# Optimization experiments

Hardware: AMD Instinct MI355X
Metric: run time of the kernel (lower is better)

## Reference

```python
import jax, jax.numpy as jnp
import numpy as np

B, N, M, F, K = 32, 256, 64, 128, 64
N_INTERACT_RES, N_ATOM_RES = 3, 2


def ssp(x):
    # shifted softplus, PhysNet activation
    return jax.nn.softplus(x) - jnp.log(2.0).astype(x.dtype)


def res_block(h, W1, b1, W2, b2):
    # PhysNet residual layer: h + W2 @ ssp(W1 @ ssp(h) + b1) + b2
    t = ssp(h)
    t = ssp(t @ W1.T + b1)
    return h + t @ W2.T + b2


def setup_inputs() -> dict:
    key = jax.random.key(0)
    ks = jax.random.split(key, 20)
    sF = 1.0 / np.sqrt(F)
    sK = 1.0 / np.sqrt(K)
    return {
        "x": jax.random.normal(ks[0], (B, N, F), jnp.float32),
        "rbf": jax.random.uniform(ks[1], (B, N, M, K), jnp.float32),
        "neighbor": jax.random.randint(ks[2], (B, N, M), 0, N, jnp.int32),
        "k2f_W": jax.random.normal(ks[3], (F, K), jnp.float32) * sK,  # no bias
        "Wi": jax.random.normal(ks[4], (F, F), jnp.float32) * sF,
        "bi": jnp.zeros((F,), jnp.float32),
        "ires_W1": jax.random.normal(ks[5], (N_INTERACT_RES, F, F), jnp.float32) * sF,
        "ires_b1": jnp.zeros((N_INTERACT_RES, F), jnp.float32),
        "ires_W2": jax.random.normal(ks[6], (N_INTERACT_RES, F, F), jnp.float32) * sF,
        "ires_b2": jnp.zeros((N_INTERACT_RES, F), jnp.float32),
        "Wint": jax.random.normal(ks[7], (F, F), jnp.float32) * sF,
        "bint": jnp.zeros((F,), jnp.float32),
        "u_gate": jnp.ones((F,), jnp.float32),
        "ares_W1": jax.random.normal(ks[8], (N_ATOM_RES, F, F), jnp.float32) * sF,
        "ares_b1": jnp.zeros((N_ATOM_RES, F), jnp.float32),
        "ares_W2": jax.random.normal(ks[9], (N_ATOM_RES, F, F), jnp.float32) * sF,
        "ares_b2": jnp.zeros((N_ATOM_RES, F), jnp.float32),
    }


def reference(x, rbf, neighbor, k2f_W, Wi, bi, ires_W1, ires_b1, ires_W2, ires_b2,
              Wint, bint, u_gate, ares_W1, ares_b1, ares_W2, ares_b2):
    b, n, f = x.shape
    m = neighbor.shape[2]
    xa = ssp(x)                                            # (B,N,F)
    g = jnp.einsum('bnmk,fk->bnmf', rbf, k2f_W)            # RBF filter (B,N,M,F)
    xi = ssp(xa @ Wi.T + bi)                               # self message
    # gather neighbor features: xj[b,n,m,:] = xa[b, neighbor[b,n,m], :]
    idx = jnp.broadcast_to(neighbor.reshape(b, n * m)[:, :, None], (b, n * m, f))
    xj = jnp.take_along_axis(xa, idx, axis=1).reshape(b, n, m, f)
    xj = jnp.sum(xj * g, axis=2)                           # aggregate over neighbors
    v = xi + xj
    for l in range(ires_W1.shape[0]):
        v = res_block(v, ires_W1[l], ires_b1[l], ires_W2[l], ires_b2[l])
    v = ssp(v)
    out = u_gate * x + (v @ Wint.T + bint)
    for l in range(ares_W1.shape[0]):
        out = res_block(out, ares_W1[l], ares_b1[l], ares_W2[l], ares_b2[l])
    return out
```

## Files before the change

### kernel.cpp

```cpp
#include <hip/hip_runtime.h>
#include <math.h>

#define PB 32
#define PN 256
#define PM 64
#define PF 128
#define PK 64
#define ROWS (PB*PN)
#define NTOT (ROWS*PF)

#define OFF_K2F  0
#define OFF_WI   8192
#define OFF_IW1  24576
#define OFF_IW2  73728
#define OFF_WINT 122880
#define OFF_AW1  139264
#define OFF_AW2  172032
#define TOTAL_W  204800

#define XPITCH 136
#define GPITCH 132

#define APB 32

typedef __attribute__((ext_vector_type(4))) float  floatx4;
typedef __attribute__((ext_vector_type(8))) short  shortx8;

__device__ __forceinline__ unsigned short f2b(float f){
    union { float f; unsigned int i; } c; c.f = f;
    unsigned int x = c.i;
    return (unsigned short)((x + 0x7fffu + ((x >> 16) & 1u)) >> 16);
}
__device__ __forceinline__ float sspf(float x){
    const float LOG2E = 1.4426950408889634f;
    const float LN2   = 0.6931471805599453f;
    float t = __builtin_amdgcn_exp2f(-fabsf(x) * LOG2E);
    return fmaxf(x, 0.0f) + LN2 * __builtin_amdgcn_logf(1.0f + t) - LN2;
}
__device__ __forceinline__ shortx8 pack8(float4 a, float4 b){
    shortx8 r;
    r[0]=(short)f2b(a.x); r[1]=(short)f2b(a.y); r[2]=(short)f2b(a.z); r[3]=(short)f2b(a.w);
    r[4]=(short)f2b(b.x); r[5]=(short)f2b(b.y); r[6]=(short)f2b(b.z); r[7]=(short)f2b(b.w);
    return r;
}

__global__ __launch_bounds__(256) void k_pre(const float* __restrict__ x,
                                             const float* __restrict__ k2f,
                                             const float* __restrict__ Wi,
                                             const float* __restrict__ iW1,
                                             const float* __restrict__ iW2,
                                             const float* __restrict__ Wint,
                                             const float* __restrict__ aW1,
                                             const float* __restrict__ aW2,
                                             float* __restrict__ xa_f,
                                             unsigned short* __restrict__ xa_b,
                                             unsigned short* __restrict__ Wb){
    int i = blockIdx.x * 256 + threadIdx.x;
    if (i < NTOT){
        float v = sspf(x[i]);
        xa_f[i] = v;
        xa_b[i] = f2b(v);
        return;
    }
    int j = i - NTOT;
    if (j >= TOTAL_W) return;
    float v;
    if      (j < OFF_WI)   v = k2f[j - OFF_K2F];
    else if (j < OFF_IW1)  v = Wi[j - OFF_WI];
    else if (j < OFF_IW2)  v = iW1[j - OFF_IW1];
    else if (j < OFF_WINT) v = iW2[j - OFF_IW2];
    else if (j < OFF_AW1)  v = Wint[j - OFF_WINT];
    else if (j < OFF_AW2)  v = aW1[j - OFF_AW1];
    else                   v = aW2[j - OFF_AW2];
    Wb[j] = f2b(v);
}

__global__ __launch_bounds__(512, 2) void k_msg(const float* __restrict__ rbf,
                                                const int* __restrict__ nbr,
                                                const unsigned short* __restrict__ Wk2f,
                                                const float* __restrict__ xa_f,
                                                float* __restrict__ xj){
    const int tid  = threadIdx.x;
    const int w    = tid >> 6;
    const int lane = tid & 63;
    const int quad = lane >> 4;
    const int l16  = lane & 15;

    const int blk   = blockIdx.x;
    const int b     = blk >> 3;
    const int atom0 = b * PN + (blk & 7) * APB;
    const int awave = atom0 + w*4;

    __shared__ float          xa_s[PN * GPITCH];
    __shared__ unsigned short w_s[8192];

    const int rboff = l16 * PK + quad*8;
    const float* rb_base = rbf + (size_t)awave * (PM*PK);
    const int*   nb_base = nbr + (size_t)awave * PM + quad*4;

    float4 r0, r1, r2, r3; int4 nb;
    {
        const float* p0 = rb_base + rboff;
        r0 = *(const float4*)(p0);
        r1 = *(const float4*)(p0 + 4);
        r2 = *(const float4*)(p0 + 32);
        r3 = *(const float4*)(p0 + 36);
        nb = *(const int4*)(nb_base);
    }

    #pragma unroll
    for (int rep = 0; rep < 2; ++rep){
        int f  = rep*512 + tid;
        int s  = f >> 9;
        int ft = (f >> 6) & 7;
        int ln = f & 63;
        const unsigned short* g = Wk2f + (size_t)(ft*16 + (ln & 15))*PK + s*32 + (ln >> 4)*8;
        *(shortx8*)(&w_s[f*8]) = *(const shortx8*)(g);
    }

    const float* src = xa_f + (size_t)b * (PN*PF);
    #pragma unroll
    for (int p = 0; p < 16; ++p){
        int idx = p*2048 + tid*4;
        int row = idx >> 7, col = idx & 127;
        *(float4*)(&xa_s[row*GPITCH + col]) = *(const float4*)(src + idx);
    }
    __syncthreads();

    float s[8];
    #pragma unroll
    for (int it = 0; it < 16; ++it){
        const int ai = it >> 2;
        const int t  = it & 3;

        shortx8 af0 = pack8(r0, r1);
        shortx8 af1 = pack8(r2, r3);
        const int4 nbc = nb;

        if (it + 1 < 16){
            const int it2 = it + 1;
            const int ai2 = it2 >> 2, t2 = it2 & 3;
            const float* pn = rb_base + (size_t)ai2*(PM*PK) + t2*16*PK + rboff;
            r0 = *(const float4*)(pn);
            r1 = *(const float4*)(pn + 4);
            r2 = *(const float4*)(pn + 32);
            r3 = *(const float4*)(pn + 36);
            nb = *(const int4*)(nb_base + (size_t)ai2*PM + t2*16);
        }

        const float* rp0 = xa_s + (size_t)nbc.x*GPITCH + l16;
        const float* rp1 = xa_s + (size_t)nbc.y*GPITCH + l16;
        const float* rp2 = xa_s + (size_t)nbc.z*GPITCH + l16;
        const float* rp3 = xa_s + (size_t)nbc.w*GPITCH + l16;

        #pragma unroll
        for (int ft = 0; ft < 8; ++ft){
            shortx8 b0 = *(const shortx8*)(&w_s[(ft*64 + lane)*8]);
            shortx8 b1 = *(const shortx8*)(&w_s[((8 + ft)*64 + lane)*8]);
            floatx4 c = {0.f, 0.f, 0.f, 0.f};
            c = __builtin_amdgcn_mfma_f32_16x16x32_bf16(af0, b0, c, 0, 0, 0);
            c = __builtin_amdgcn_mfma_f32_16x16x32_bf16(af1, b1, c, 0, 0, 0);
            float v =  c[0] * rp0[ft*16];
            v       += c[1] * rp1[ft*16];
            v       += c[2] * rp2[ft*16];
            v       += c[3] * rp3[ft*16];
            if (t == 0) s[ft] = v; else s[ft] += v;
        }

        if (t == 3){
            #pragma unroll
            for (int ft = 0; ft < 8; ++ft){
                float v = s[ft];
                v += __shfl_xor(v, 16, 64);
                v += __shfl_xor(v, 32, 64);
                if (quad == 0) xj[(size_t)(awave + ai)*PF + ft*16 + l16] = v;
            }
        }
    }
}

__device__ __forceinline__ void lw8(const unsigned short* __restrict__ W,
                                    int l16, int quad, int ftb, shortx8 wf[8]){
    #pragma unroll
    for (int f = 0; f < 2; ++f)
        #pragma unroll
        for (int ks = 0; ks < 4; ++ks)
            wf[f*4+ks] = *(const shortx8*)(W + (size_t)((ftb+f)*16 + l16)*PF + ks*32 + quad*8);
}
__device__ __forceinline__ void gemm2p(const shortx8 wf[8], const shortx8 a[4], floatx4 acc[2]){
    #pragma unroll
    for (int f = 0; f < 2; ++f){
        floatx4 c = {0.f, 0.f, 0.f, 0.f};
        #pragma unroll
        for (int ks = 0; ks < 4; ++ks)
            c = __builtin_amdgcn_mfma_f32_16x16x32_bf16(a[ks], wf[f*4+ks], c, 0, 0, 0);
        acc[f] = c;
    }
}

__device__ __forceinline__ void relayout(unsigned short* Tls,
                                         const unsigned short t16[8],
                                         int l16, int quad, int ftbase,
                                         shortx8 a[4]){
    #pragma unroll
    for (int f = 0; f < 2; ++f)
        #pragma unroll
        for (int r = 0; r < 4; ++r)
            Tls[(quad*4 + r)*XPITCH + (ftbase+f)*16 + l16] = t16[f*4 + r];
    __syncthreads();
    #pragma unroll
    for (int ks = 0; ks < 4; ++ks)
        a[ks] = *(const shortx8*)(Tls + l16*XPITCH + ks*32 + quad*8);
}

__global__ __launch_bounds__(256) void k_chain(const unsigned short* __restrict__ xa_b,
                                               const float* __restrict__ xj,
                                               const float* __restrict__ x,
                                               const unsigned short* __restrict__ Wb,
                                               const float* __restrict__ bi,
                                               const float* __restrict__ ib1,
                                               const float* __restrict__ ib2,
                                               const float* __restrict__ bint,
                                               const float* __restrict__ ugate,
                                               const float* __restrict__ ab1,
                                               const float* __restrict__ ab2,
                                               float* __restrict__ out){
    const int tid  = threadIdx.x;
    const int wave = tid >> 6;
    const int lane = tid & 63;
    const int quad = lane >> 4;
    const int l16  = lane & 15;
    const int ftb  = wave*2;
    const int row0 = blockIdx.x * 16;

    __shared__ unsigned short Tls[2][16 * XPITCH];
    int p = 0;

    int col[2];
    #pragma unroll
    for (int f = 0; f < 2; ++f) col[f] = (ftb+f)*16 + l16;

    const unsigned short* inrow = xa_b + (size_t)(row0 + l16) * PF;
    shortx8 a[4];
    #pragma unroll
    for (int ks = 0; ks < 4; ++ks)
        a[ks] = *(const shortx8*)(inrow + ks*32 + quad*8);

    shortx8 wA[8], wB[8];
    lw8(Wb + OFF_WI, l16, quad, ftb, wA);

    floatx4 acc[2];
    float V[8];
    unsigned short t16[8];

    lw8(Wb + OFF_IW1, l16, quad, ftb, wB);
    gemm2p(wA, a, acc);
    #pragma unroll
    for (int f = 0; f < 2; ++f)
        #pragma unroll
        for (int r = 0; r < 4; ++r){
            size_t idx = (size_t)(row0 + quad*4 + r)*PF + col[f];
            float of = sspf(acc[f][r] + bi[col[f]]) + xj[idx];
            V[f*4+r] = of;
            t16[f*4+r] = f2b(sspf(of));
        }
    relayout(Tls[p], t16, l16, quad, ftb, a); p ^= 1;

    #pragma unroll
    for (int l = 0; l < 3; ++l){
        lw8(Wb + OFF_IW2 + l*PF*PF, l16, quad, ftb, wA);
        gemm2p(wB, a, acc);
        #pragma unroll
        for (int f = 0; f < 2; ++f)
            #pragma unroll
            for (int r = 0; r < 4; ++r)
                t16[f*4+r] = f2b(sspf(acc[f][r] + ib1[l*PF + col[f]]));
        relayout(Tls[p], t16, l16, quad, ftb, a); p ^= 1;

        lw8(Wb + (l < 2 ? OFF_IW1 + (l+1)*PF*PF : OFF_WINT), l16, quad, ftb, wB);
        gemm2p(wA, a, acc);
        #pragma unroll
        for (int f = 0; f < 2; ++f)
            #pragma unroll
            for (int r = 0; r < 4; ++r){
                V[f*4+r] += acc[f][r] + ib2[l*PF + col[f]];
                t16[f*4+r] = f2b(sspf(V[f*4+r]));
            }
        relayout(Tls[p], t16, l16, quad, ftb, a); p ^= 1;
    }

    lw8(Wb + OFF_AW1, l16, quad, ftb, wA);
    gemm2p(wB, a, acc);
    #pragma unroll
    for (int f = 0; f < 2; ++f)
        #pragma unroll
        for (int r = 0; r < 4; ++r){
            size_t idx = (size_t)(row0 + quad*4 + r)*PF + col[f];
            float o = ugate[col[f]] * x[idx] + acc[f][r] + bint[col[f]];
            V[f*4+r] = o;
            t16[f*4+r] = f2b(sspf(o));
        }
    relayout(Tls[p], t16, l16, quad, ftb, a); p ^= 1;

    #pragma unroll
    for (int l = 0; l < 2; ++l){
        lw8(Wb + OFF_AW2 + l*PF*PF, l16, quad, ftb, wB);
        gemm2p(wA, a, acc);
        #pragma unroll
        for (int f = 0; f < 2; ++f)
            #pragma unroll
            for (int r = 0; r < 4; ++r)
                t16[f*4+r] = f2b(sspf(acc[f][r] + ab1[l*PF + col[f]]));
        relayout(Tls[p], t16, l16, quad, ftb, a); p ^= 1;

        if (l == 0) lw8(Wb + OFF_AW1 + PF*PF, l16, quad, ftb, wA);
        gemm2p(wB, a, acc);
        if (l == 0){
            #pragma unroll
            for (int f = 0; f < 2; ++f)
                #pragma unroll
                for (int r = 0; r < 4; ++r){
                    V[f*4+r] += acc[f][r] + ab2[l*PF + col[f]];
                    t16[f*4+r] = f2b(sspf(V[f*4+r]));
                }
            relayout(Tls[p], t16, l16, quad, ftb, a); p ^= 1;
        } else {
            #pragma unroll
            for (int f = 0; f < 2; ++f)
                #pragma unroll
                for (int r = 0; r < 4; ++r){
                    size_t idx = (size_t)(row0 + quad*4 + r)*PF + col[f];
                    out[idx] = V[f*4+r] + acc[f][r] + ab2[l*PF + col[f]];
                }
        }
    }
}

extern "C" void kernel_launch(void* const* d_in, const int* in_sizes, int n_in,
                              void* d_out, int out_size, void* d_ws, size_t ws_size,
                              hipStream_t stream){
    const float* x     = (const float*)d_in[0];
    const float* rbf   = (const float*)d_in[1];
    const int*   nbr   = (const int*)d_in[2];
    const float* k2fW  = (const float*)d_in[3];
    const float* Wi    = (const float*)d_in[4];
    const float* bi    = (const float*)d_in[5];
    const float* iW1   = (const float*)d_in[6];
    const float* ib1   = (const float*)d_in[7];
    const float* iW2   = (const float*)d_in[8];
    const float* ib2   = (const float*)d_in[9];
    const float* Wint  = (const float*)d_in[10];
    const float* bint  = (const float*)d_in[11];
    const float* ugate = (const float*)d_in[12];
    const float* aW1   = (const float*)d_in[13];
    const float* ab1   = (const float*)d_in[14];
    const float* aW2   = (const float*)d_in[15];
    const float* ab2   = (const float*)d_in[16];

    char* ws = (char*)d_ws;
    unsigned short* xa_b = (unsigned short*)ws;
    float*          xa_f = (float*)(ws + (2ull  << 20));
    float*          xj   = (float*)(ws + (6ull  << 20));
    unsigned short* Wb   = (unsigned short*)(ws + (10ull << 20));

    k_pre<<<(NTOT + TOTAL_W + 255)/256, 256, 0, stream>>>(
        x, k2fW, Wi, iW1, iW2, Wint, aW1, aW2, xa_f, xa_b, Wb);
    k_msg<<<PB * (PN/APB), 512, 0, stream>>>(rbf, nbr, Wb + OFF_K2F, xa_f, xj);
    k_chain<<<ROWS/16, 256, 0, stream>>>(xa_b, xj, x, Wb,
                                         bi, ib1, ib2, bint, ugate, ab1, ab2,
                                         (float*)d_out);
}
```

Baseline: 272.4 us.

## Gather neighbor features from global memory and shrink message kernel blocks to one atom per wave

The message kernel no longer stages each molecule's full activation table (about 135 KB) in LDS. It gathers neighbor rows straight from global memory, relying on L2/L1 caching. Blocks drop to 256 threads with one atom per wave, giving 2048 blocks instead of 256, and RBF tiles are double-buffered two steps ahead. The aim is to remove the large per-block LDS fill and raise occupancy, at the cost of uncoalesced global gathers and reloading the weight tile in every small block.

```diff
diff --git a/kernel.cpp b/kernel.cpp
--- a/kernel.cpp
+++ b/kernel.cpp
@@ -19,9 +19,6 @@
 #define TOTAL_W  204800
 
 #define XPITCH 136
-#define GPITCH 132
-
-#define APB 32
 
 typedef __attribute__((ext_vector_type(4))) float  floatx4;
 typedef __attribute__((ext_vector_type(8))) short  shortx8;
@@ -75,7 +72,7 @@
     Wb[j] = f2b(v);
 }
 
-__global__ __launch_bounds__(512, 2) void k_msg(const float* __restrict__ rbf,
+__global__ __launch_bounds__(256, 4) void k_msg(const float* __restrict__ rbf,
                                                 const int* __restrict__ nbr,
                                                 const unsigned short* __restrict__ Wk2f,
                                                 const float* __restrict__ xa_f,
@@ -86,96 +83,95 @@
     const int quad = lane >> 4;
     const int l16  = lane & 15;
 
-    const int blk   = blockIdx.x;
-    const int b     = blk >> 3;
-    const int atom0 = b * PN + (blk & 7) * APB;
-    const int awave = atom0 + w*4;
-
-    __shared__ float          xa_s[PN * GPITCH];
+    const int atom = blockIdx.x * 4 + w;
+    const int b    = atom >> 8;
+
     __shared__ unsigned short w_s[8192];
 
     const int rboff = l16 * PK + quad*8;
-    const float* rb_base = rbf + (size_t)awave * (PM*PK);
-    const int*   nb_base = nbr + (size_t)awave * PM + quad*4;
-
-    float4 r0, r1, r2, r3; int4 nb;
+    const float* rb_base = rbf + (size_t)atom * (PM*PK);
+    const int*   nb_base = nbr + (size_t)atom * PM + quad*4;
+    const float* xab     = xa_f + (size_t)b * (PN*PF) + l16;
+
+    float4 a0,a1,a2,a3, b0v,b1v,b2v,b3v;
+    int4 nbA, nbB;
     {
         const float* p0 = rb_base + rboff;
-        r0 = *(const float4*)(p0);
-        r1 = *(const float4*)(p0 + 4);
-        r2 = *(const float4*)(p0 + 32);
-        r3 = *(const float4*)(p0 + 36);
-        nb = *(const int4*)(nb_base);
-    }
-
-    #pragma unroll
-    for (int rep = 0; rep < 2; ++rep){
-        int f  = rep*512 + tid;
+        a0 = *(const float4*)(p0);
+        a1 = *(const float4*)(p0 + 4);
+        a2 = *(const float4*)(p0 + 32);
+        a3 = *(const float4*)(p0 + 36);
+        nbA = *(const int4*)(nb_base);
+        const float* p1 = rb_base + 16*PK + rboff;
+        b0v = *(const float4*)(p1);
+        b1v = *(const float4*)(p1 + 4);
+        b2v = *(const float4*)(p1 + 32);
+        b3v = *(const float4*)(p1 + 36);
+        nbB = *(const int4*)(nb_base + 16);
+    }
+
+    #pragma unroll
+    for (int rep = 0; rep < 4; ++rep){
+        int f  = rep*256 + tid;
         int s  = f >> 9;
         int ft = (f >> 6) & 7;
         int ln = f & 63;
         const unsigned short* g = Wk2f + (size_t)(ft*16 + (ln & 15))*PK + s*32 + (ln >> 4)*8;
         *(shortx8*)(&w_s[f*8]) = *(const shortx8*)(g);
     }
-
-    const float* src = xa_f + (size_t)b * (PN*PF);
-    #pragma unroll
-    for (int p = 0; p < 16; ++p){
-        int idx = p*2048 + tid*4;
-        int row = idx >> 7, col = idx & 127;
-        *(float4*)(&xa_s[row*GPITCH + col]) = *(const float4*)(src + idx);
-    }
     __syncthreads();
 
     float s[8];
     #pragma unroll
-    for (int it = 0; it < 16; ++it){
-        const int ai = it >> 2;
-        const int t  = it & 3;
-
-        shortx8 af0 = pack8(r0, r1);
-        shortx8 af1 = pack8(r2, r3);
-        const int4 nbc = nb;
-
-        if (it + 1 < 16){
-            const int it2 = it + 1;
-            const int ai2 = it2 >> 2, t2 = it2 & 3;
-            const float* pn = rb_base + (size_t)ai2*(PM*PK) + t2*16*PK + rboff;
-            r0 = *(const float4*)(pn);
-            r1 = *(const float4*)(pn + 4);
-            r2 = *(const float4*)(pn + 32);
-            r3 = *(const float4*)(pn + 36);
-            nb = *(const int4*)(nb_base + (size_t)ai2*PM + t2*16);
-        }
-
-        const float* rp0 = xa_s + (size_t)nbc.x*GPITCH + l16;
-        const float* rp1 = xa_s + (size_t)nbc.y*GPITCH + l16;
-        const float* rp2 = xa_s + (size_t)nbc.z*GPITCH + l16;
-        const float* rp3 = xa_s + (size_t)nbc.w*GPITCH + l16;
+    for (int t = 0; t < 4; ++t){
+        shortx8 af0, af1; int4 nbc;
+        if ((t & 1) == 0){ af0 = pack8(a0, a1);  af1 = pack8(a2, a3);  nbc = nbA; }
+        else             { af0 = pack8(b0v, b1v); af1 = pack8(b2v, b3v); nbc = nbB; }
+
+        if (t + 2 < 4){
+            const float* pn = rb_base + (t+2)*16*PK + rboff;
+            const int4*  nn = (const int4*)(nb_base + (t+2)*16);
+            if ((t & 1) == 0){
+                a0 = *(const float4*)(pn);
+                a1 = *(const float4*)(pn + 4);
+                a2 = *(const float4*)(pn + 32);
+                a3 = *(const float4*)(pn + 36);
+                nbA = *nn;
+            } else {
+                b0v = *(const float4*)(pn);
+                b1v = *(const float4*)(pn + 4);
+                b2v = *(const float4*)(pn + 32);
+                b3v = *(const float4*)(pn + 36);
+                nbB = *nn;
+            }
+        }
+
+        const float* rp0 = xab + (size_t)nbc.x * PF;
+        const float* rp1 = xab + (size_t)nbc.y * PF;
+        const float* rp2 = xab + (size_t)nbc.z * PF;
+        const float* rp3 = xab + (size_t)nbc.w * PF;
 
         #pragma unroll
         for (int ft = 0; ft < 8; ++ft){
-            shortx8 b0 = *(const shortx8*)(&w_s[(ft*64 + lane)*8]);
-            shortx8 b1 = *(const shortx8*)(&w_s[((8 + ft)*64 + lane)*8]);
+            shortx8 w0 = *(const shortx8*)(&w_s[(ft*64 + lane)*8]);
+            shortx8 w1 = *(const shortx8*)(&w_s[((8 + ft)*64 + lane)*8]);
             floatx4 c = {0.f, 0.f, 0.f, 0.f};
-            c = __builtin_amdgcn_mfma_f32_16x16x32_bf16(af0, b0, c, 0, 0, 0);
-            c = __builtin_amdgcn_mfma_f32_16x16x32_bf16(af1, b1, c, 0, 0, 0);
+            c = __builtin_amdgcn_mfma_f32_16x16x32_bf16(af0, w0, c, 0, 0, 0);
+            c = __builtin_amdgcn_mfma_f32_16x16x32_bf16(af1, w1, c, 0, 0, 0);
             float v =  c[0] * rp0[ft*16];
             v       += c[1] * rp1[ft*16];
             v       += c[2] * rp2[ft*16];
             v       += c[3] * rp3[ft*16];
             if (t == 0) s[ft] = v; else s[ft] += v;
         }
-
-        if (t == 3){
-            #pragma unroll
-            for (int ft = 0; ft < 8; ++ft){
-                float v = s[ft];
-                v += __shfl_xor(v, 16, 64);
-                v += __shfl_xor(v, 32, 64);
-                if (quad == 0) xj[(size_t)(awave + ai)*PF + ft*16 + l16] = v;
-            }
-        }
+    }
+
+    #pragma unroll
+    for (int ft = 0; ft < 8; ++ft){
+        float v = s[ft];
+        v += __shfl_xor(v, 16, 64);
+        v += __shfl_xor(v, 32, 64);
+        if (quad == 0) xj[(size_t)atom*PF + ft*16 + l16] = v;
     }
 }
 
@@ -365,7 +361,7 @@
 
     k_pre<<<(NTOT + TOTAL_W + 255)/256, 256, 0, stream>>>(
         x, k2fW, Wi, iW1, iW2, Wint, aW1, aW2, xa_f, xa_b, Wb);
-    k_msg<<<PB * (PN/APB), 512, 0, stream>>>(rbf, nbr, Wb + OFF_K2F, xa_f, xj);
+    k_msg<<<ROWS/4, 256, 0, stream>>>(rbf, nbr, Wb + OFF_K2F, xa_f, xj);
     k_chain<<<ROWS/16, 256, 0, stream>>>(xa_b, xj, x, Wb,
                                          bi, ib1, ib2, bint, ugate, ab1, ab2,
                                          (float*)d_out);
```

New measurement: 337.9 us. +24.0%, slower.
